# Optimization experiments

Measured on AMD Instinct MI355X. Metric: run time of the kernel, lower is better.

## Reference

```python
import jax, jax.numpy as jnp
import numpy as np

B, L, H = 2, 2048, 1024
E = H * 2          # mamba_dim = model_dim * expansion_factor
K = 4              # conv kernel size
N = 16             # SSM state dim
DT_RANK = H // 8   # 128, mamba default ceil(d_model/16) scaled on d_inner


def setup_inputs() -> dict:
    key = jax.random.key(0)
    ks = jax.random.split(key, 12)
    s = lambda fan_in: 1.0 / np.sqrt(fan_in)
    return {
        "x": jax.random.normal(ks[0], (B, L, H), jnp.float32),
        "W_in": jax.random.normal(ks[1], (H, 2 * E), jnp.float32) * s(H),
        "b_in": jnp.zeros((2 * E,), jnp.float32),
        "conv_w": jax.random.normal(ks[2], (E, 1, K), jnp.float32) * s(K),  # depthwise OIH
        "conv_b": jnp.zeros((E,), jnp.float32),
        "x_proj_w": jax.random.normal(ks[3], (E, DT_RANK + 2 * N), jnp.float32) * s(E),
        "dt_proj_w": jax.random.normal(ks[4], (DT_RANK, E), jnp.float32) * s(DT_RANK),
        "dt_bias": jax.random.uniform(ks[5], (E,), jnp.float32, -4.0, -2.0),  # softplus(.) small
        "A_log": jnp.log(jnp.broadcast_to(jnp.arange(1, N + 1, dtype=jnp.float32), (E, N))),
        "D_param": jnp.ones((E,), jnp.float32),
        "W_out": jax.random.normal(ks[6], (E, H), jnp.float32) * s(E),
        "b_out": jnp.zeros((H,), jnp.float32),
    }


def _selective_scan(u, delta, A, Bm, Cm, Dp):
    # u, delta: (B,L,E); A: (E,N); Bm, Cm: (B,L,N); Dp: (E,)
    def step(h, inp):
        d_t, u_t, b_t, c_t = inp          # (B,E), (B,E), (B,N), (B,N)
        dA = jnp.exp(d_t[..., None] * A)  # (B,E,N)
        h = dA * h + (d_t * u_t)[..., None] * b_t[:, None, :]
        y = jnp.einsum("ben,bn->be", h, c_t)
        return h, y

    h0 = jnp.zeros((u.shape[0], A.shape[0], A.shape[1]), u.dtype)
    xs = (delta.transpose(1, 0, 2), u.transpose(1, 0, 2),
          Bm.transpose(1, 0, 2), Cm.transpose(1, 0, 2))
    _, ys = jax.lax.scan(step, h0, xs)    # ys: (L,B,E)
    return ys.transpose(1, 0, 2) + u * Dp


def reference(x, W_in, b_in, conv_w, conv_b, x_proj_w, dt_proj_w, dt_bias,
              A_log, D_param, W_out, b_out):
    silu = jax.nn.silu
    z = x @ W_in + b_in                    # (B,L,2E)
    xc, xr = z[..., :E], z[..., E:]
    xr = silu(xr)
    # causal depthwise conv1d: left-pad K-1 (== torch pad=K-1 then truncate to L)
    xt = xc.transpose(0, 2, 1)             # (B,E,L)
    xt = jax.lax.conv_general_dilated(
        xt, conv_w, window_strides=(1,), padding=[(K - 1, 0)],
        feature_group_count=E, dimension_numbers=("NCH", "OIH", "NCH"))
    xc = silu((xt + conv_b[None, :, None]).transpose(0, 2, 1))  # (B,L,E)
    # S6 selective SSM
    proj = xc @ x_proj_w                   # (B,L,dt_rank+2N)
    dt = proj[..., :DT_RANK]
    Bm = proj[..., DT_RANK:DT_RANK + N]
    Cm = proj[..., DT_RANK + N:]
    delta = jax.nn.softplus(dt @ dt_proj_w + dt_bias)  # (B,L,E)
    A = -jnp.exp(A_log)                    # (E,N)
    y = _selective_scan(xc, delta, A, Bm, Cm, D_param)
    y = y * xr                             # gate
    return y @ W_out + b_out
```

## Files before the change

### kernel.cpp

```cpp
#include <hip/hip_runtime.h>
#include <cstdint>

#define SL 2048
#define SE 2048
#define SB 2
#define SN 16
#define SC 64
#define ST 32

enum { EP_SPLIT_SILU = 1, EP_SOFTPLUS = 2, EP_BIAS = 3, EP_PARTIAL = 4 };

typedef __attribute__((ext_vector_type(8))) short bf16x8;
typedef __attribute__((ext_vector_type(4))) float f32x4;

__device__ __forceinline__ float silu_f(float x) { return x / (1.f + __expf(-x)); }
__device__ __forceinline__ float softplus_f(float x) {
    return (x > 20.f) ? x : log1pf(__expf(x));
}
__device__ __forceinline__ ushort f2bf(float f) {
    union { float f; unsigned u; } a; a.f = f;
    unsigned r = a.u + 0x7fff + ((a.u >> 16) & 1);
    return (ushort)(r >> 16);
}
__device__ __forceinline__ void gload16(const void* g, void* l) {
    __builtin_amdgcn_global_load_lds(
        (const __attribute__((address_space(1))) unsigned int*)g,
        (__attribute__((address_space(3))) unsigned int*)l, 16, 0, 0);
}

template <int MODE>
__global__ __launch_bounds__(256, 2) void hgemm2(
    const ushort* __restrict__ A, const ushort* __restrict__ Bt,
    float* __restrict__ C, const float* __restrict__ bias,
    float* __restrict__ out2, int M, int N, int K, int Esplit, int KS)
{
    __shared__ ushort As[2][128 * 64];
    __shared__ ushort Bs[2][128 * 64];
    const int tid = threadIdx.x;
    const int w = tid >> 6, l = tid & 63;
    const int wr = w >> 1, wc = w & 1;
    const int m0 = blockIdx.y * 128, n0 = blockIdx.x * 128;
    const int z = blockIdx.z;
    const int kbeg = z * KS;
    const int nt = KS / 64;
    const int srow = l >> 3, scol = (l & 7) * 8;

    f32x4 acc[4][4];
#pragma unroll
    for (int m = 0; m < 4; m++)
#pragma unroll
        for (int n = 0; n < 4; n++) acc[m][n] = (f32x4)(0.f);

    auto stage = [&](int buf, int t) {
        const int k0 = kbeg + t * 64;
#pragma unroll
        for (int r = 0; r < 4; r++) {
            const int row = r * 32 + w * 8 + srow;
            int brow = n0 + row; if (brow > N - 1) brow = N - 1;
            gload16(A + (size_t)(m0 + row) * K + k0 + scol,
                    &As[buf][r * 2048 + w * 512]);
            gload16(Bt + (size_t)brow * K + k0 + scol,
                    &Bs[buf][r * 2048 + w * 512]);
        }
    };

    stage(0, 0);
    __syncthreads();

    int cur = 0;
    const int fr = l & 15, kc = (l >> 4) * 8;
    for (int t = 0; t < nt; t++) {
        if (t + 1 < nt) stage(cur ^ 1, t + 1);
#pragma unroll
        for (int kk = 0; kk < 64; kk += 32) {
            bf16x8 af[4], bfr[4];
#pragma unroll
            for (int m = 0; m < 4; m++)
                af[m] = *(const bf16x8*)&As[cur][(wr * 64 + m * 16 + fr) * 64 + kk + kc];
#pragma unroll
            for (int n = 0; n < 4; n++)
                bfr[n] = *(const bf16x8*)&Bs[cur][(wc * 64 + n * 16 + fr) * 64 + kk + kc];
#pragma unroll
            for (int m = 0; m < 4; m++)
#pragma unroll
                for (int n = 0; n < 4; n++)
                    acc[m][n] = __builtin_amdgcn_mfma_f32_16x16x32_bf16(
                        af[m], bfr[n], acc[m][n], 0, 0, 0);
        }
        __syncthreads();
        cur ^= 1;
    }

    const int cr = (l >> 4) * 4, cc = l & 15;
    float* pbase = C + (size_t)z * M * N;
#pragma unroll
    for (int m = 0; m < 4; m++) {
#pragma unroll
        for (int j = 0; j < 4; j++) {
            const int row = m0 + wr * 64 + m * 16 + cr + j;
#pragma unroll
            for (int n = 0; n < 4; n++) {
                const int col = n0 + wc * 64 + n * 16 + cc;
                float v = acc[m][n][j];
                if (MODE == EP_SPLIT_SILU) {
                    v += bias[col];
                    if (col < Esplit)
                        C[(size_t)row * Esplit + col] = v;
                    else
                        out2[(size_t)row * Esplit + (col - Esplit)] = silu_f(v);
                } else if (MODE == EP_SOFTPLUS) {
                    C[(size_t)row * N + col] = softplus_f(v + bias[col]);
                } else if (MODE == EP_BIAS) {
                    C[(size_t)row * N + col] = v + bias[col];
                } else {
                    if (col < N) pbase[(size_t)row * N + col] = v;
                }
            }
        }
    }
}

__global__ __launch_bounds__(256) void gemm3_reduce(
    const float* __restrict__ Pp, float* __restrict__ proj,
    ushort* __restrict__ dtbf, int M, int N, int Z)
{
    const size_t g = (size_t)blockIdx.x * 256 + threadIdx.x;
    const size_t tot = (size_t)M * N;
    if (g >= tot) return;
    float s = 0.f;
    for (int z = 0; z < Z; z++) s += Pp[(size_t)z * tot + g];
    proj[g] = s;
    const int col = (int)(g % N);
    if (col < 128) {
        const size_t row = g / N;
        dtbf[row * 128 + col] = f2bf(s);
    }
}

__global__ __launch_bounds__(256) void reduce6(
    const float* __restrict__ Pp, const float* __restrict__ bias,
    float* __restrict__ out, int M, int N)
{
    const size_t g = (size_t)blockIdx.x * 256 + threadIdx.x;
    const size_t tot = (size_t)M * N;
    if (g >= tot) return;
    out[g] = Pp[g] + Pp[tot + g] + bias[g % N];
}

__global__ __launch_bounds__(256) void f2bf_vec(
    const float* __restrict__ in, ushort* __restrict__ out, size_t n4)
{
    for (size_t i = (size_t)blockIdx.x * 256 + threadIdx.x; i < n4;
         i += (size_t)gridDim.x * 256) {
        float4 v = ((const float4*)in)[i];
        ushort4 o;
        o.x = f2bf(v.x); o.y = f2bf(v.y); o.z = f2bf(v.z); o.w = f2bf(v.w);
        ((ushort4*)out)[i] = o;
    }
}

__global__ __launch_bounds__(256) void f2bf_transpose(
    const float* __restrict__ W, ushort* __restrict__ Wt, int R, int Ccols)
{
    __shared__ float tile[32][33];
    const int bc = blockIdx.x * 32, br = blockIdx.y * 32;
    const int tx = threadIdx.x & 31, ty = threadIdx.x >> 5;
    for (int i = ty; i < 32; i += 8)
        tile[i][tx] = W[(size_t)(br + i) * Ccols + bc + tx];
    __syncthreads();
    for (int i = ty; i < 32; i += 8)
        Wt[(size_t)(bc + i) * R + br + tx] = f2bf(tile[tx][i]);
}

__global__ __launch_bounds__(256) void conv_silu4(
    const float* __restrict__ xin, const float* __restrict__ w,
    const float* __restrict__ cb, float* __restrict__ xo,
    ushort* __restrict__ xobf, int Ln, int En, size_t total4)
{
    const int Eq = En >> 2;
    for (size_t idx = (size_t)blockIdx.x * 256 + threadIdx.x; idx < total4;
         idx += (size_t)gridDim.x * 256) {
        const int e4 = (int)(idx % Eq);
        const size_t row = idx / Eq;
        const int l = (int)(row % Ln);
        float4 acc = ((const float4*)cb)[e4];
        const float4 w0 = ((const float4*)w)[e4 * 4 + 0];
        const float4 w1 = ((const float4*)w)[e4 * 4 + 1];
        const float4 w2 = ((const float4*)w)[e4 * 4 + 2];
        const float4 w3 = ((const float4*)w)[e4 * 4 + 3];
        const float wt0[4] = {w0.x, w0.y, w0.z, w0.w};
        const float wt1[4] = {w1.x, w1.y, w1.z, w1.w};
        const float wt2[4] = {w2.x, w2.y, w2.z, w2.w};
        const float wt3[4] = {w3.x, w3.y, w3.z, w3.w};
#pragma unroll
        for (int k = 0; k < 4; k++) {
            if (l - 3 + k >= 0) {
                float4 xv = ((const float4*)xin)[(row - 3 + k) * Eq + e4];
                acc.x = fmaf(wt0[k], xv.x, acc.x);
                acc.y = fmaf(wt1[k], xv.y, acc.y);
                acc.z = fmaf(wt2[k], xv.z, acc.z);
                acc.w = fmaf(wt3[k], xv.w, acc.w);
            }
        }
        float4 v;
        v.x = silu_f(acc.x); v.y = silu_f(acc.y);
        v.z = silu_f(acc.z); v.w = silu_f(acc.w);
        ((float4*)xo)[idx] = v;
        ushort4 o;
        o.x = f2bf(v.x); o.y = f2bf(v.y); o.z = f2bf(v.z); o.w = f2bf(v.w);
        ((ushort4*)xobf)[idx] = o;
    }
}

__global__ __launch_bounds__(256) void scan_pass1(
    const float* __restrict__ delta, const float* __restrict__ u,
    const float* __restrict__ proj, const float* __restrict__ A_log,
    float* __restrict__ Pbuf, float* __restrict__ Sbuf)
{
    __shared__ float sB[ST * SN];
    const int tid = threadIdx.x;
    const int eb = blockIdx.x & 7;
    const int c  = (blockIdx.x >> 3) & (SC - 1);
    const int b  = blockIdx.x >> 9;
    const int e  = eb * 256 + tid;
    const size_t row0 = (size_t)b * SL + c * ST;

    for (int i = tid; i < ST * SN; i += 256) {
        const int tl = i >> 4, n = i & 15;
        sB[i] = proj[(row0 + tl) * 160 + 128 + n];
    }
    __syncthreads();

    float An[SN], h[SN];
    {
        const float4* Ap = (const float4*)(A_log + (size_t)e * SN);
#pragma unroll
        for (int q = 0; q < 4; q++) {
            float4 v = Ap[q];
            An[q * 4 + 0] = -expf(v.x);
            An[q * 4 + 1] = -expf(v.y);
            An[q * 4 + 2] = -expf(v.z);
            An[q * 4 + 3] = -expf(v.w);
        }
    }
#pragma unroll
    for (int n = 0; n < SN; n++) h[n] = 0.f;

    float dsum = 0.f;
    size_t idx = row0 * SE + e;
    float d = delta[idx], uu = u[idx];
    for (int tl = 0; tl < ST; tl++) {
        float dn = 0.f, un = 0.f;
        if (tl + 1 < ST) { dn = delta[idx + SE]; un = u[idx + SE]; }
        const float du = d * uu;
        dsum += d;
#pragma unroll
        for (int n = 0; n < SN; n++) {
            const float dA = __expf(d * An[n]);
            h[n] = fmaf(dA, h[n], du * sB[tl * SN + n]);
        }
        d = dn; uu = un; idx += SE;
    }

    const size_t ob = ((((size_t)c * SB) + b) * SE + e) * SN;
#pragma unroll
    for (int q = 0; q < 4; q++) {
        float4 pv, sv;
        pv.x = __expf(An[q * 4 + 0] * dsum); sv.x = h[q * 4 + 0];
        pv.y = __expf(An[q * 4 + 1] * dsum); sv.y = h[q * 4 + 1];
        pv.z = __expf(An[q * 4 + 2] * dsum); sv.z = h[q * 4 + 2];
        pv.w = __expf(An[q * 4 + 3] * dsum); sv.w = h[q * 4 + 3];
        *(float4*)(Pbuf + ob + q * 4) = pv;
        *(float4*)(Sbuf + ob + q * 4) = sv;
    }
}

__global__ __launch_bounds__(256) void scan_pass2(
    const float* __restrict__ Pbuf, const float* __restrict__ Sbuf,
    float* __restrict__ hinit)
{
    const size_t g = (size_t)blockIdx.x * 256 + threadIdx.x;
    const size_t stride = (size_t)SB * SE * SN;
    float h = 0.f;
    float P = Pbuf[g], S = Sbuf[g];
    for (int c = 0; c < SC; c++) {
        float Pn = 0.f, Sn = 0.f;
        if (c + 1 < SC) {
            Pn = Pbuf[(c + 1) * stride + g];
            Sn = Sbuf[(c + 1) * stride + g];
        }
        hinit[c * stride + g] = h;
        h = fmaf(P, h, S);
        P = Pn; S = Sn;
    }
}

__global__ __launch_bounds__(256) void scan_pass3(
    const float* __restrict__ delta, const float* __restrict__ u,
    const float* __restrict__ proj, const float* __restrict__ A_log,
    const float* __restrict__ Dp, const float* __restrict__ xr,
    const float* __restrict__ hinit, ushort* __restrict__ yg)
{
    __shared__ float sB[ST * SN];
    __shared__ float sC[ST * SN];
    const int tid = threadIdx.x;
    const int eb = blockIdx.x & 7;
    const int c  = (blockIdx.x >> 3) & (SC - 1);
    const int b  = blockIdx.x >> 9;
    const int e  = eb * 256 + tid;
    const size_t row0 = (size_t)b * SL + c * ST;

    for (int i = tid; i < ST * SN; i += 256) {
        const int tl = i >> 4, n = i & 15;
        sB[i] = proj[(row0 + tl) * 160 + 128 + n];
        sC[i] = proj[(row0 + tl) * 160 + 144 + n];
    }
    __syncthreads();

    float An[SN], h[SN];
    {
        const float4* Ap = (const float4*)(A_log + (size_t)e * SN);
#pragma unroll
        for (int q = 0; q < 4; q++) {
            float4 v = Ap[q];
            An[q * 4 + 0] = -expf(v.x);
            An[q * 4 + 1] = -expf(v.y);
            An[q * 4 + 2] = -expf(v.z);
            An[q * 4 + 3] = -expf(v.w);
        }
    }
    {
        const size_t ib = ((((size_t)c * SB) + b) * SE + e) * SN;
#pragma unroll
        for (int q = 0; q < 4; q++) {
            float4 v = *(const float4*)(hinit + ib + q * 4);
            h[q * 4 + 0] = v.x; h[q * 4 + 1] = v.y;
            h[q * 4 + 2] = v.z; h[q * 4 + 3] = v.w;
        }
    }
    const float De = Dp[e];

    size_t idx = row0 * SE + e;
    float d = delta[idx], uu = u[idx], g = xr[idx];
    for (int tl = 0; tl < ST; tl++) {
        float dn = 0.f, un = 0.f, gn = 0.f;
        if (tl + 1 < ST) {
            dn = delta[idx + SE]; un = u[idx + SE]; gn = xr[idx + SE];
        }
        const float du = d * uu;
        float y = 0.f;
#pragma unroll
        for (int n = 0; n < SN; n++) {
            const float dA = __expf(d * An[n]);
            h[n] = fmaf(dA, h[n], du * sB[tl * SN + n]);
            y = fmaf(h[n], sC[tl * SN + n], y);
        }
        yg[idx] = f2bf((y + uu * De) * g);
        d = dn; uu = un; g = gn; idx += SE;
    }
}

extern "C" void kernel_launch(void* const* d_in, const int* in_sizes, int n_in,
                              void* d_out, int out_size, void* d_ws, size_t ws_size,
                              hipStream_t stream)
{
    const int Bc = 2, Lc = 2048, Hc = 1024, Ec = 2048;
    const int M = Bc * Lc;
    const int PN = 160;
    const int SKZ = 8;

    const float* x        = (const float*)d_in[0];
    const float* W_in     = (const float*)d_in[1];
    const float* b_in     = (const float*)d_in[2];
    const float* conv_w   = (const float*)d_in[3];
    const float* conv_b   = (const float*)d_in[4];
    const float* x_proj_w = (const float*)d_in[5];
    const float* dt_proj_w= (const float*)d_in[6];
    const float* dt_bias  = (const float*)d_in[7];
    const float* A_log    = (const float*)d_in[8];
    const float* D_param  = (const float*)d_in[9];
    const float* W_out    = (const float*)d_in[10];
    const float* b_out    = (const float*)d_in[11];
    float* out = (float*)d_out;

    float* ws = (float*)d_ws;
    const size_t ME = (size_t)M * Ec;
    const size_t PS = (size_t)SB * SE * SC * SN;

    float* xc_raw = ws;
    float* xr     = xc_raw + ME;
    float* xc     = xr + ME;
    float* delta  = xc + ME;
    float* proj   = delta + ME;
    float* hinit  = proj + (size_t)M * PN;

    ushort* xbf    = (ushort*)delta;
    ushort* W_in_t = (ushort*)xc;
    ushort* xc_bf  = (ushort*)delta;
    float*  Pp3    = xc_raw;
    ushort* xpw_t  = (ushort*)hinit;
    ushort* dtw_t  = (ushort*)hinit + 327680;
    ushort* dtbf   = (ushort*)hinit + 327680 + 262144;
    float*  Pbuf   = xc_raw;
    float*  Sbuf   = xc_raw + PS;
    ushort* ygbf   = (ushort*)xc_raw;
    ushort* W_out_t= (ushort*)delta;
    float*  Pp6    = xr;

    f2bf_vec<<<1024, 256, 0, stream>>>(x, xbf, (size_t)M * Hc / 4);
    f2bf_transpose<<<dim3(2 * Ec / 32, Hc / 32), 256, 0, stream>>>(
        W_in, W_in_t, Hc, 2 * Ec);
    f2bf_transpose<<<dim3(PN / 32, Ec / 32), 256, 0, stream>>>(
        x_proj_w, xpw_t, Ec, PN);
    f2bf_transpose<<<dim3(Ec / 32, 128 / 32), 256, 0, stream>>>(
        dt_proj_w, dtw_t, 128, Ec);

    hgemm2<EP_SPLIT_SILU><<<dim3(2 * Ec / 128, M / 128, 1), 256, 0, stream>>>(
        xbf, W_in_t, xc_raw, b_in, xr, M, 2 * Ec, Hc, Ec, Hc);

    conv_silu4<<<2048, 256, 0, stream>>>(
        xc_raw, conv_w, conv_b, xc, xc_bf, Lc, Ec, ME / 4);

    hgemm2<EP_PARTIAL><<<dim3(2, M / 128, SKZ), 256, 0, stream>>>(
        xc_bf, xpw_t, Pp3, nullptr, nullptr, M, PN, Ec, 0, Ec / SKZ);
    gemm3_reduce<<<(M * PN + 255) / 256, 256, 0, stream>>>(
        Pp3, proj, dtbf, M, PN, SKZ);

    hgemm2<EP_SOFTPLUS><<<dim3(Ec / 128, M / 128, 1), 256, 0, stream>>>(
        dtbf, dtw_t, delta, dt_bias, nullptr, M, Ec, 128, 0, 128);

    scan_pass1<<<SB * SC * (SE / 256), 256, 0, stream>>>(
        delta, xc, proj, A_log, Pbuf, Sbuf);
    scan_pass2<<<(SB * SE * SN) / 256, 256, 0, stream>>>(Pbuf, Sbuf, hinit);
    scan_pass3<<<SB * SC * (SE / 256), 256, 0, stream>>>(
        delta, xc, proj, A_log, D_param, xr, hinit, ygbf);

    f2bf_transpose<<<dim3(Hc / 32, Ec / 32), 256, 0, stream>>>(
        W_out, W_out_t, Ec, Hc);

    hgemm2<EP_PARTIAL><<<dim3(Hc / 128, M / 128, 2), 256, 0, stream>>>(
        ygbf, W_out_t, Pp6, nullptr, nullptr, M, Hc, Ec, 0, Ec / 2);
    reduce6<<<(M * Hc + 255) / 256, 256, 0, stream>>>(Pp6, b_out, out, M, Hc);
}
```

Before: 345.8 us.

## Add 256x256-tile 512-thread GEMM for in/out projections, raise out-proj split-K

Adds an hgemm256 kernel that uses 256x256 output tiles, K-steps of 32 and 8 waves per block. It replaces the 128x128 GEMM for the input projection (split+SiLU epilogue) and for the output projection. The larger tiles raise operand reuse per LDS load and give about one block per CU. The output projection moves from split-K 2 to split-K 4 to keep enough blocks in flight, and reduce6 is vectorised with float4 to sum any number of partials plus the bias. The risk is that four partial buffers need twice the workspace previously aliased onto xr, which may overrun into adjacent buffers. The shorter K-step also means more barriers per unit of work.

```diff
diff --git a/kernel.cpp b/kernel.cpp
--- a/kernel.cpp
+++ b/kernel.cpp
@@ -26,6 +26,93 @@
     __builtin_amdgcn_global_load_lds(
         (const __attribute__((address_space(1))) unsigned int*)g,
         (__attribute__((address_space(3))) unsigned int*)l, 16, 0, 0);
+}
+
+template <int MODE>
+__global__ __launch_bounds__(512, 2) void hgemm256(
+    const ushort* __restrict__ A, const ushort* __restrict__ Bt,
+    float* __restrict__ C, const float* __restrict__ bias,
+    float* __restrict__ out2, int M, int N, int K, int Esplit, int KS)
+{
+    __shared__ ushort As[2][256 * 32];
+    __shared__ ushort Bs[2][256 * 32];
+    const int tid = threadIdx.x;
+    const int w = tid >> 6, l = tid & 63;
+    const int wr = w >> 2, wc = w & 3;
+    const int m0 = blockIdx.y * 256, n0 = blockIdx.x * 256;
+    const int z = blockIdx.z;
+    const int kbeg = z * KS;
+    const int nt = KS / 32;
+    const int srow = l >> 2;
+    const int scol = (l & 3) * 8;
+
+    f32x4 acc[8][4];
+#pragma unroll
+    for (int m = 0; m < 8; m++)
+#pragma unroll
+        for (int n = 0; n < 4; n++) acc[m][n] = (f32x4)(0.f);
+
+    auto stage = [&](int buf, int t) {
+        const int k0 = kbeg + t * 32;
+#pragma unroll
+        for (int r = 0; r < 2; r++) {
+            const int row = w * 32 + r * 16 + srow;
+            gload16(A + (size_t)(m0 + row) * K + k0 + scol,
+                    &As[buf][(w * 32 + r * 16) * 32]);
+            gload16(Bt + (size_t)(n0 + row) * K + k0 + scol,
+                    &Bs[buf][(w * 32 + r * 16) * 32]);
+        }
+    };
+
+    stage(0, 0);
+    __syncthreads();
+
+    int cur = 0;
+    const int fr = l & 15, kc = (l >> 4) * 8;
+    for (int t = 0; t < nt; t++) {
+        if (t + 1 < nt) stage(cur ^ 1, t + 1);
+        bf16x8 af[8], bfr[4];
+#pragma unroll
+        for (int m = 0; m < 8; m++)
+            af[m] = *(const bf16x8*)&As[cur][(wr * 128 + m * 16 + fr) * 32 + kc];
+#pragma unroll
+        for (int n = 0; n < 4; n++)
+            bfr[n] = *(const bf16x8*)&Bs[cur][(wc * 64 + n * 16 + fr) * 32 + kc];
+#pragma unroll
+        for (int m = 0; m < 8; m++)
+#pragma unroll
+            for (int n = 0; n < 4; n++)
+                acc[m][n] = __builtin_amdgcn_mfma_f32_16x16x32_bf16(
+                    af[m], bfr[n], acc[m][n], 0, 0, 0);
+        __syncthreads();
+        cur ^= 1;
+    }
+
+    const int cr = (l >> 4) * 4, cc = l & 15;
+    float* pbase = C + (size_t)z * M * N;
+#pragma unroll
+    for (int m = 0; m < 8; m++) {
+#pragma unroll
+        for (int j = 0; j < 4; j++) {
+            const int row = m0 + wr * 128 + m * 16 + cr + j;
+#pragma unroll
+            for (int n = 0; n < 4; n++) {
+                const int col = n0 + wc * 64 + n * 16 + cc;
+                float v = acc[m][n][j];
+                if (MODE == EP_SPLIT_SILU) {
+                    v += bias[col];
+                    if (col < Esplit)
+                        C[(size_t)row * Esplit + col] = v;
+                    else
+                        out2[(size_t)row * Esplit + (col - Esplit)] = silu_f(v);
+                } else if (MODE == EP_BIAS) {
+                    C[(size_t)row * N + col] = v + bias[col];
+                } else {
+                    pbase[(size_t)row * N + col] = v;
+                }
+            }
+        }
+    }
 }
 
 template <int MODE>
@@ -102,13 +189,7 @@
             for (int n = 0; n < 4; n++) {
                 const int col = n0 + wc * 64 + n * 16 + cc;
                 float v = acc[m][n][j];
-                if (MODE == EP_SPLIT_SILU) {
-                    v += bias[col];
-                    if (col < Esplit)
-                        C[(size_t)row * Esplit + col] = v;
-                    else
-                        out2[(size_t)row * Esplit + (col - Esplit)] = silu_f(v);
-                } else if (MODE == EP_SOFTPLUS) {
+                if (MODE == EP_SOFTPLUS) {
                     C[(size_t)row * N + col] = softplus_f(v + bias[col]);
                 } else if (MODE == EP_BIAS) {
                     C[(size_t)row * N + col] = v + bias[col];
@@ -139,12 +220,18 @@
 
 __global__ __launch_bounds__(256) void reduce6(
     const float* __restrict__ Pp, const float* __restrict__ bias,
-    float* __restrict__ out, int M, int N)
+    float* __restrict__ out, int M, int N, int Z)
 {
     const size_t g = (size_t)blockIdx.x * 256 + threadIdx.x;
-    const size_t tot = (size_t)M * N;
-    if (g >= tot) return;
-    out[g] = Pp[g] + Pp[tot + g] + bias[g % N];
+    const size_t tot4 = (size_t)M * N / 4;
+    if (g >= tot4) return;
+    const int n4 = N / 4;
+    float4 s = ((const float4*)bias)[g % n4];
+    for (int z = 0; z < Z; z++) {
+        float4 p = ((const float4*)Pp)[z * tot4 + g];
+        s.x += p.x; s.y += p.y; s.z += p.z; s.w += p.w;
+    }
+    ((float4*)out)[g] = s;
 }
 
 __global__ __launch_bounds__(256) void f2bf_vec(
@@ -368,6 +455,7 @@
     const int M = Bc * Lc;
     const int PN = 160;
     const int SKZ = 8;
+    const int SK6 = 4;
 
     const float* x        = (const float*)d_in[0];
     const float* W_in     = (const float*)d_in[1];
@@ -415,7 +503,7 @@
     f2bf_transpose<<<dim3(Ec / 32, 128 / 32), 256, 0, stream>>>(
         dt_proj_w, dtw_t, 128, Ec);
 
-    hgemm2<EP_SPLIT_SILU><<<dim3(2 * Ec / 128, M / 128, 1), 256, 0, stream>>>(
+    hgemm256<EP_SPLIT_SILU><<<dim3(2 * Ec / 256, M / 256, 1), 512, 0, stream>>>(
         xbf, W_in_t, xc_raw, b_in, xr, M, 2 * Ec, Hc, Ec, Hc);
 
     conv_silu4<<<2048, 256, 0, stream>>>(
@@ -438,7 +526,8 @@
     f2bf_transpose<<<dim3(Hc / 32, Ec / 32), 256, 0, stream>>>(
         W_out, W_out_t, Ec, Hc);
 
-    hgemm2<EP_PARTIAL><<<dim3(Hc / 128, M / 128, 2), 256, 0, stream>>>(
-        ygbf, W_out_t, Pp6, nullptr, nullptr, M, Hc, Ec, 0, Ec / 2);
-    reduce6<<<(M * Hc + 255) / 256, 256, 0, stream>>>(Pp6, b_out, out, M, Hc);
-}
+    hgemm256<EP_PARTIAL><<<dim3(Hc / 256, M / 256, SK6), 512, 0, stream>>>(
+        ygbf, W_out_t, Pp6, nullptr, nullptr, M, Hc, Ec, 0, Ec / SK6);
+    reduce6<<<(int)((size_t)M * Hc / 4 + 255) / 256, 256, 0, stream>>>(
+        Pp6, b_out, out, M, Hc, SK6);
+}
```

New measurement: 368.2 us. +6.5%, slower.

## Fold dt_proj into x_proj weight and fuse delta/BC projection into one GEMM

Applied to the files above, without the earlier changes.

Precomputes the combined weight x_proj_w[:, :128] @ dt_proj_w in bf16, so delta comes from a single GEMM over xc with a 2048+32 wide output that also emits B and C. This removes the split-K x_proj GEMM, its reduction kernel and the separate dt_proj GEMM, and drops the fp32 xc buffer so the scans read bf16 u. The single GEMM does more FLOPs (K=2048, N=2080 instead of a rank-128 path) and rounds the combined weight to bf16, which changes numerics slightly. reduce6 is also vectorised with float4.

```diff
diff --git a/kernel.cpp b/kernel.cpp
--- a/kernel.cpp
+++ b/kernel.cpp
@@ -8,7 +8,7 @@
 #define SC 64
 #define ST 32
 
-enum { EP_SPLIT_SILU = 1, EP_SOFTPLUS = 2, EP_BIAS = 3, EP_PARTIAL = 4 };
+enum { EP_SPLIT_SILU = 1, EP_PARTIAL = 4, EP_BF16 = 5, EP_FUSED34 = 6 };
 
 typedef __attribute__((ext_vector_type(8))) short bf16x8;
 typedef __attribute__((ext_vector_type(4))) float f32x4;
@@ -22,6 +22,10 @@
     unsigned r = a.u + 0x7fff + ((a.u >> 16) & 1);
     return (ushort)(r >> 16);
 }
+__device__ __forceinline__ float bf2f(ushort u) {
+    union { float f; unsigned u; } a; a.u = ((unsigned)u) << 16;
+    return a.f;
+}
 __device__ __forceinline__ void gload16(const void* g, void* l) {
     __builtin_amdgcn_global_load_lds(
         (const __attribute__((address_space(1))) unsigned int*)g,
@@ -32,7 +36,8 @@
 __global__ __launch_bounds__(256, 2) void hgemm2(
     const ushort* __restrict__ A, const ushort* __restrict__ Bt,
     float* __restrict__ C, const float* __restrict__ bias,
-    float* __restrict__ out2, int M, int N, int K, int Esplit, int KS)
+    float* __restrict__ out2, ushort* __restrict__ outu,
+    int M, int N, int K, int Esplit, int KS)
 {
     __shared__ ushort As[2][128 * 64];
     __shared__ ushort Bs[2][128 * 64];
@@ -108,10 +113,13 @@
                         C[(size_t)row * Esplit + col] = v;
                     else
                         out2[(size_t)row * Esplit + (col - Esplit)] = silu_f(v);
-                } else if (MODE == EP_SOFTPLUS) {
-                    C[(size_t)row * N + col] = softplus_f(v + bias[col]);
-                } else if (MODE == EP_BIAS) {
-                    C[(size_t)row * N + col] = v + bias[col];
+                } else if (MODE == EP_FUSED34) {
+                    if (col < Esplit)
+                        C[(size_t)row * Esplit + col] = softplus_f(v + bias[col]);
+                    else if (col < N)
+                        out2[(size_t)row * 32 + (col - Esplit)] = v;
+                } else if (MODE == EP_BF16) {
+                    outu[(size_t)row * N + col] = f2bf(v);
                 } else {
                     if (col < N) pbase[(size_t)row * N + col] = v;
                 }
@@ -120,31 +128,20 @@
     }
 }
 
-__global__ __launch_bounds__(256) void gemm3_reduce(
-    const float* __restrict__ Pp, float* __restrict__ proj,
-    ushort* __restrict__ dtbf, int M, int N, int Z)
-{
-    const size_t g = (size_t)blockIdx.x * 256 + threadIdx.x;
-    const size_t tot = (size_t)M * N;
-    if (g >= tot) return;
-    float s = 0.f;
-    for (int z = 0; z < Z; z++) s += Pp[(size_t)z * tot + g];
-    proj[g] = s;
-    const int col = (int)(g % N);
-    if (col < 128) {
-        const size_t row = g / N;
-        dtbf[row * 128 + col] = f2bf(s);
-    }
-}
-
 __global__ __launch_bounds__(256) void reduce6(
     const float* __restrict__ Pp, const float* __restrict__ bias,
-    float* __restrict__ out, int M, int N)
+    float* __restrict__ out, int M, int N, int Z)
 {
     const size_t g = (size_t)blockIdx.x * 256 + threadIdx.x;
-    const size_t tot = (size_t)M * N;
-    if (g >= tot) return;
-    out[g] = Pp[g] + Pp[tot + g] + bias[g % N];
+    const size_t tot4 = (size_t)M * N / 4;
+    if (g >= tot4) return;
+    const int n4 = N / 4;
+    float4 s = ((const float4*)bias)[g % n4];
+    for (int z = 0; z < Z; z++) {
+        float4 p = ((const float4*)Pp)[z * tot4 + g];
+        s.x += p.x; s.y += p.y; s.z += p.z; s.w += p.w;
+    }
+    ((float4*)out)[g] = s;
 }
 
 __global__ __launch_bounds__(256) void f2bf_vec(
@@ -172,10 +169,36 @@
         Wt[(size_t)(bc + i) * R + br + tx] = f2bf(tile[tx][i]);
 }
 
+__global__ __launch_bounds__(256) void cast_xpw128(
+    const float* __restrict__ W, ushort* __restrict__ out)
+{
+    const int idx = blockIdx.x * 256 + threadIdx.x;
+    if (idx >= 2048 * 32) return;
+    const int row = idx >> 5;
+    const int c4 = (idx & 31) * 4;
+    const float4 v = *(const float4*)&W[(size_t)row * 160 + c4];
+    ushort4 o;
+    o.x = f2bf(v.x); o.y = f2bf(v.y); o.z = f2bf(v.z); o.w = f2bf(v.w);
+    *(ushort4*)&out[(size_t)row * 128 + c4] = o;
+}
+
+__global__ __launch_bounds__(256) void bc_weight_t(
+    const float* __restrict__ W, ushort* __restrict__ Wt)
+{
+    __shared__ float tile[32][33];
+    const int br = blockIdx.y * 32;
+    const int tx = threadIdx.x & 31, ty = threadIdx.x >> 5;
+    for (int i = ty; i < 32; i += 8)
+        tile[i][tx] = W[(size_t)(br + i) * 160 + 128 + tx];
+    __syncthreads();
+    for (int i = ty; i < 32; i += 8)
+        Wt[(size_t)i * 2048 + br + tx] = f2bf(tile[tx][i]);
+}
+
 __global__ __launch_bounds__(256) void conv_silu4(
     const float* __restrict__ xin, const float* __restrict__ w,
-    const float* __restrict__ cb, float* __restrict__ xo,
-    ushort* __restrict__ xobf, int Ln, int En, size_t total4)
+    const float* __restrict__ cb, ushort* __restrict__ xobf,
+    int Ln, int En, size_t total4)
 {
     const int Eq = En >> 2;
     for (size_t idx = (size_t)blockIdx.x * 256 + threadIdx.x; idx < total4;
@@ -202,19 +225,16 @@
                 acc.w = fmaf(wt3[k], xv.w, acc.w);
             }
         }
-        float4 v;
-        v.x = silu_f(acc.x); v.y = silu_f(acc.y);
-        v.z = silu_f(acc.z); v.w = silu_f(acc.w);
-        ((float4*)xo)[idx] = v;
         ushort4 o;
-        o.x = f2bf(v.x); o.y = f2bf(v.y); o.z = f2bf(v.z); o.w = f2bf(v.w);
+        o.x = f2bf(silu_f(acc.x)); o.y = f2bf(silu_f(acc.y));
+        o.z = f2bf(silu_f(acc.z)); o.w = f2bf(silu_f(acc.w));
         ((ushort4*)xobf)[idx] = o;
     }
 }
 
 __global__ __launch_bounds__(256) void scan_pass1(
-    const float* __restrict__ delta, const float* __restrict__ u,
-    const float* __restrict__ proj, const float* __restrict__ A_log,
+    const float* __restrict__ delta, const ushort* __restrict__ u,
+    const float* __restrict__ BC, const float* __restrict__ A_log,
     float* __restrict__ Pbuf, float* __restrict__ Sbuf)
 {
     __shared__ float sB[ST * SN];
@@ -225,10 +245,8 @@
     const int e  = eb * 256 + tid;
     const size_t row0 = (size_t)b * SL + c * ST;
 
-    for (int i = tid; i < ST * SN; i += 256) {
-        const int tl = i >> 4, n = i & 15;
-        sB[i] = proj[(row0 + tl) * 160 + 128 + n];
-    }
+    for (int i = tid; i < ST * SN; i += 256)
+        sB[i] = BC[(row0 + (i >> 4)) * 32 + (i & 15)];
     __syncthreads();
 
     float An[SN], h[SN];
@@ -248,10 +266,10 @@
 
     float dsum = 0.f;
     size_t idx = row0 * SE + e;
-    float d = delta[idx], uu = u[idx];
+    float d = delta[idx], uu = bf2f(u[idx]);
     for (int tl = 0; tl < ST; tl++) {
         float dn = 0.f, un = 0.f;
-        if (tl + 1 < ST) { dn = delta[idx + SE]; un = u[idx + SE]; }
+        if (tl + 1 < ST) { dn = delta[idx + SE]; un = bf2f(u[idx + SE]); }
         const float du = d * uu;
         dsum += d;
 #pragma unroll
@@ -296,8 +314,8 @@
 }
 
 __global__ __launch_bounds__(256) void scan_pass3(
-    const float* __restrict__ delta, const float* __restrict__ u,
-    const float* __restrict__ proj, const float* __restrict__ A_log,
+    const float* __restrict__ delta, const ushort* __restrict__ u,
+    const float* __restrict__ BC, const float* __restrict__ A_log,
     const float* __restrict__ Dp, const float* __restrict__ xr,
     const float* __restrict__ hinit, ushort* __restrict__ yg)
 {
@@ -311,9 +329,8 @@
     const size_t row0 = (size_t)b * SL + c * ST;
 
     for (int i = tid; i < ST * SN; i += 256) {
-        const int tl = i >> 4, n = i & 15;
-        sB[i] = proj[(row0 + tl) * 160 + 128 + n];
-        sC[i] = proj[(row0 + tl) * 160 + 144 + n];
+        sB[i] = BC[(row0 + (i >> 4)) * 32 + (i & 15)];
+        sC[i] = BC[(row0 + (i >> 4)) * 32 + 16 + (i & 15)];
     }
     __syncthreads();
 
@@ -341,11 +358,11 @@
     const float De = Dp[e];
 
     size_t idx = row0 * SE + e;
-    float d = delta[idx], uu = u[idx], g = xr[idx];
+    float d = delta[idx], uu = bf2f(u[idx]), g = xr[idx];
     for (int tl = 0; tl < ST; tl++) {
         float dn = 0.f, un = 0.f, gn = 0.f;
         if (tl + 1 < ST) {
-            dn = delta[idx + SE]; un = u[idx + SE]; gn = xr[idx + SE];
+            dn = delta[idx + SE]; un = bf2f(u[idx + SE]); gn = xr[idx + SE];
         }
         const float du = d * uu;
         float y = 0.f;
@@ -366,8 +383,8 @@
 {
     const int Bc = 2, Lc = 2048, Hc = 1024, Ec = 2048;
     const int M = Bc * Lc;
-    const int PN = 160;
-    const int SKZ = 8;
+    const int NF = 2080;
+    const int SK6 = 2;
 
     const float* x        = (const float*)d_in[0];
     const float* W_in     = (const float*)d_in[1];
@@ -389,18 +406,17 @@
 
     float* xc_raw = ws;
     float* xr     = xc_raw + ME;
-    float* xc     = xr + ME;
-    float* delta  = xc + ME;
-    float* proj   = delta + ME;
-    float* hinit  = proj + (size_t)M * PN;
+    float* r2     = xr + ME;
+    float* delta  = r2 + ME / 2;
+    float* hinit  = delta + ME;
+    ushort* Wbig  = (ushort*)(hinit + PS);
+    float* BC     = (float*)(Wbig + (size_t)2176 * 2048);
+    ushort* xpw128= (ushort*)(BC + (size_t)M * 32);
+    ushort* dtw_t = xpw128 + (size_t)2048 * 128;
 
     ushort* xbf    = (ushort*)delta;
-    ushort* W_in_t = (ushort*)xc;
-    ushort* xc_bf  = (ushort*)delta;
-    float*  Pp3    = xc_raw;
-    ushort* xpw_t  = (ushort*)hinit;
-    ushort* dtw_t  = (ushort*)hinit + 327680;
-    ushort* dtbf   = (ushort*)hinit + 327680 + 262144;
+    ushort* W_in_t = (ushort*)r2;
+    ushort* xc_bf  = (ushort*)r2;
     float*  Pbuf   = xc_raw;
     float*  Sbuf   = xc_raw + PS;
     ushort* ygbf   = (ushort*)xc_raw;
@@ -410,35 +426,35 @@
     f2bf_vec<<<1024, 256, 0, stream>>>(x, xbf, (size_t)M * Hc / 4);
     f2bf_transpose<<<dim3(2 * Ec / 32, Hc / 32), 256, 0, stream>>>(
         W_in, W_in_t, Hc, 2 * Ec);
-    f2bf_transpose<<<dim3(PN / 32, Ec / 32), 256, 0, stream>>>(
-        x_proj_w, xpw_t, Ec, PN);
+    cast_xpw128<<<256, 256, 0, stream>>>(x_proj_w, xpw128);
     f2bf_transpose<<<dim3(Ec / 32, 128 / 32), 256, 0, stream>>>(
         dt_proj_w, dtw_t, 128, Ec);
+    bc_weight_t<<<dim3(1, Ec / 32), 256, 0, stream>>>(
+        x_proj_w, Wbig + (size_t)2048 * 2048);
+
+    hgemm2<EP_BF16><<<dim3(16, 16, 1), 256, 0, stream>>>(
+        dtw_t, xpw128, nullptr, nullptr, nullptr, Wbig, 2048, 2048, 128, 0, 128);
 
     hgemm2<EP_SPLIT_SILU><<<dim3(2 * Ec / 128, M / 128, 1), 256, 0, stream>>>(
-        xbf, W_in_t, xc_raw, b_in, xr, M, 2 * Ec, Hc, Ec, Hc);
+        xbf, W_in_t, xc_raw, b_in, xr, nullptr, M, 2 * Ec, Hc, Ec, Hc);
 
     conv_silu4<<<2048, 256, 0, stream>>>(
-        xc_raw, conv_w, conv_b, xc, xc_bf, Lc, Ec, ME / 4);
-
-    hgemm2<EP_PARTIAL><<<dim3(2, M / 128, SKZ), 256, 0, stream>>>(
-        xc_bf, xpw_t, Pp3, nullptr, nullptr, M, PN, Ec, 0, Ec / SKZ);
-    gemm3_reduce<<<(M * PN + 255) / 256, 256, 0, stream>>>(
-        Pp3, proj, dtbf, M, PN, SKZ);
-
-    hgemm2<EP_SOFTPLUS><<<dim3(Ec / 128, M / 128, 1), 256, 0, stream>>>(
-        dtbf, dtw_t, delta, dt_bias, nullptr, M, Ec, 128, 0, 128);
+        xc_raw, conv_w, conv_b, xc_bf, Lc, Ec, ME / 4);
+
+    hgemm2<EP_FUSED34><<<dim3((NF + 127) / 128, M / 128, 1), 256, 0, stream>>>(
+        xc_bf, Wbig, delta, dt_bias, BC, nullptr, M, NF, Ec, Ec, Ec);
 
     scan_pass1<<<SB * SC * (SE / 256), 256, 0, stream>>>(
-        delta, xc, proj, A_log, Pbuf, Sbuf);
+        delta, xc_bf, BC, A_log, Pbuf, Sbuf);
     scan_pass2<<<(SB * SE * SN) / 256, 256, 0, stream>>>(Pbuf, Sbuf, hinit);
     scan_pass3<<<SB * SC * (SE / 256), 256, 0, stream>>>(
-        delta, xc, proj, A_log, D_param, xr, hinit, ygbf);
+        delta, xc_bf, BC, A_log, D_param, xr, hinit, ygbf);
 
     f2bf_transpose<<<dim3(Hc / 32, Ec / 32), 256, 0, stream>>>(
         W_out, W_out_t, Ec, Hc);
 
-    hgemm2<EP_PARTIAL><<<dim3(Hc / 128, M / 128, 2), 256, 0, stream>>>(
-        ygbf, W_out_t, Pp6, nullptr, nullptr, M, Hc, Ec, 0, Ec / 2);
-    reduce6<<<(M * Hc + 255) / 256, 256, 0, stream>>>(Pp6, b_out, out, M, Hc);
-}
+    hgemm2<EP_PARTIAL><<<dim3(Hc / 128, M / 128, SK6), 256, 0, stream>>>(
+        ygbf, W_out_t, Pp6, nullptr, nullptr, nullptr, M, Hc, Ec, 0, Ec / SK6);
+    reduce6<<<(int)((size_t)M * Hc / 4 + 255) / 256, 256, 0, stream>>>(
+        Pp6, b_out, out, M, Hc, SK6);
+}
```

Measured after the change: 446.0 us. 29.0% more time.
